# Optimization experiments

Measured on AMD Instinct MI355X. Metric: run time of the kernel, lower is better.

## Reference

```python
import jax, jax.numpy as jnp
import numpy as np

B, D, O = 8192, 64, 256

def setup_inputs() -> dict:
    key = jax.random.key(0)
    k1, k2, k3 = jax.random.split(key, 3)
    x = jax.random.normal(k1, (B, D), dtype=jnp.float32)
    centers = jax.random.uniform(k2, (O, 1, D), dtype=jnp.float32)  # RandomUniform(0,1)
    # Original uses Constant(10.0) which saturates exp(-quad) to 0; use small random
    # betas so the quadratic form is in a numerically meaningful range.
    betas = jax.random.normal(k3, (O, D, D), dtype=jnp.float32) * 0.05
    return {"x": x, "centers": centers, "betas": betas}

def reference(x, centers, betas):
    # precision[o] = betas[o] @ betas[o]^T   -> [O, D, D]
    precision = jnp.einsum('ode,ofe->odf', betas, betas)
    # diff[o,b,:] = centers[o] - x[b]        -> [O, B, D]
    diff = centers - x[None, :, :]
    # quad[o,b] = diff[o,b]^T P[o] diff[o,b] -> [O, B]
    quad = jnp.einsum('obd,odf,obf->ob', diff, precision, diff)
    return jnp.exp(-quad).T  # [B, O]
```

## Files before the change

kernel.cpp:

```cpp
#include <hip/hip_runtime.h>
#include <hip/hip_bf16.h>

typedef __bf16 bf16x8 __attribute__((ext_vector_type(8)));
typedef __bf16 bf16x4 __attribute__((ext_vector_type(4)));
typedef float  f32x4  __attribute__((ext_vector_type(4)));

constexpr int Bn = 8192, Dn = 64, On = 256;

__global__ void k_prep_beta(const float* __restrict__ betas, const float* __restrict__ centers,
                            __bf16* __restrict__ bT, float* __restrict__ cproj) {
    __shared__ float s[64 * 65];
    const int o = blockIdx.x, tid = threadIdx.x;
    const float* bo = betas + (size_t)o * 4096;
    for (int j = tid; j < 1024; j += 256) {
        int d = j >> 4, e = (j & 15) * 4;
        float4 v = ((const float4*)bo)[j];
        s[d * 65 + e + 0] = v.x; s[d * 65 + e + 1] = v.y;
        s[d * 65 + e + 2] = v.z; s[d * 65 + e + 3] = v.w;
    }
    __syncthreads();
    for (int j = tid; j < 1024; j += 256) {
        int e = j >> 4, d = (j & 15) * 4;
        bf16x4 r;
        r[0] = (__bf16)s[(d + 0) * 65 + e]; r[1] = (__bf16)s[(d + 1) * 65 + e];
        r[2] = (__bf16)s[(d + 2) * 65 + e]; r[3] = (__bf16)s[(d + 3) * 65 + e];
        *(bf16x4*)(bT + (size_t)o * 4096 + e * 64 + d) = r;
    }
    if (tid < 64) {
        float acc = 0.f;
        for (int d = 0; d < 64; ++d) acc += s[d * 65 + tid] * centers[o * 64 + d];
        cproj[o * 64 + tid] = acc;
    }
}

__global__ __launch_bounds__(256, 3) void k_main(const float* __restrict__ x,
                                                 const __bf16* __restrict__ bT,
                                                 const float* __restrict__ cproj,
                                                 float* __restrict__ out) {
    __shared__ __align__(16) unsigned char smem[256 * 144 + 256 * 8 * 4];
    __bf16* sX = (__bf16*)smem;
    float*  sQ = (float*)(smem + 256 * 144);

    const int tid  = threadIdx.x;
    const int w    = tid >> 6, lane = tid & 63;
    const int col  = lane & 15, grp = lane >> 4;
    const int ob   = blockIdx.x;
    const int bbase = blockIdx.y * 256;

#pragma unroll
    for (int it = 0; it < 16; ++it) {
        int i = it * 256 + tid;
        int row = i >> 4, q4 = i & 15;
        float4 v = ((const float4*)(x + (size_t)(bbase + row) * 64))[q4];
        bf16x4 r;
        r[0] = (__bf16)v.x; r[1] = (__bf16)v.y; r[2] = (__bf16)v.z; r[3] = (__bf16)v.w;
        *(bf16x4*)(sX + row * 72 + q4 * 4) = r;
    }

    const int o0 = ob * 8 + w * 2;
    bf16x8 A[2][4][2];
    f32x4  cpv[2][4];
#pragma unroll
    for (int o2 = 0; o2 < 2; ++o2) {
        const __bf16* bo = bT + (size_t)(o0 + o2) * 4096 + (size_t)col * 64 + grp * 8;
        const float*  cp = cproj + (o0 + o2) * 64 + grp * 4;
#pragma unroll
        for (int mi = 0; mi < 4; ++mi) {
            A[o2][mi][0] = *(const bf16x8*)(bo + mi * 16 * 64);
            A[o2][mi][1] = *(const bf16x8*)(bo + mi * 16 * 64 + 32);
            cpv[o2][mi]  = *(const f32x4*)(cp + mi * 16);
        }
    }
    __syncthreads();

#pragma unroll
    for (int n = 0; n < 16; ++n) {
        const __bf16* xr = sX + (n * 16 + col) * 72 + grp * 8;
        bf16x8 x0 = *(const bf16x8*)(xr);
        bf16x8 x1 = *(const bf16x8*)(xr + 32);
#pragma unroll
        for (int o2 = 0; o2 < 2; ++o2) {
            f32x4 qv = {0.f, 0.f, 0.f, 0.f};
#pragma unroll
            for (int mi = 0; mi < 4; ++mi) {
                f32x4 acc = {0.f, 0.f, 0.f, 0.f};
                acc = __builtin_amdgcn_mfma_f32_16x16x32_bf16(A[o2][mi][0], x0, acc, 0, 0, 0);
                acc = __builtin_amdgcn_mfma_f32_16x16x32_bf16(A[o2][mi][1], x1, acc, 0, 0, 0);
                f32x4 t = cpv[o2][mi] - acc;
                qv += t * t;
            }
            float qs = (qv[0] + qv[1]) + (qv[2] + qv[3]);
            qs += __shfl_xor(qs, 16, 64);
            qs += __shfl_xor(qs, 32, 64);
            if (grp == o2) sQ[(n * 16 + col) * 8 + w * 2 + o2] = qs;
        }
    }
    __syncthreads();

    f32x4 q0 = *(const f32x4*)(sQ + tid * 8);
    f32x4 q1 = *(const f32x4*)(sQ + tid * 8 + 4);
    f32x4 r0, r1;
#pragma unroll
    for (int j = 0; j < 4; ++j) { r0[j] = __expf(-q0[j]); r1[j] = __expf(-q1[j]); }
    float* op = out + (size_t)(bbase + tid) * 256 + ob * 8;
    *(f32x4*)op       = r0;
    *(f32x4*)(op + 4) = r1;
}

extern "C" void kernel_launch(void* const* d_in, const int* in_sizes, int n_in,
                              void* d_out, int out_size, void* d_ws, size_t ws_size,
                              hipStream_t stream) {
    const float* x       = (const float*)d_in[0];
    const float* centers = (const float*)d_in[1];
    const float* betas   = (const float*)d_in[2];
    float* out = (float*)d_out;

    char* ws = (char*)d_ws;
    __bf16* bT  = (__bf16*)ws;
    float*  cpj = (float*)(ws + 2 * (1 << 20));

    k_prep_beta<<<dim3(On),                dim3(256), 0, stream>>>(betas, centers, bT, cpj);
    k_main     <<<dim3(On / 8, Bn / 256),  dim3(256), 0, stream>>>(x, bT, cpj, out);
}
```

Before: 90.08 us.

## Give each wave one output, fold centre projection into MFMA accumulator, drop shuffles

Each wave now handles a single output index instead of two. The negated centre projection seeds the MFMA accumulator, so the subtraction disappears. Cross-lane shuffle reductions are replaced by writing partial sums to shared memory and reducing them during the exp/store phase. The grid is reordered so the batch is the fast dimension, shared memory is reused for the partial sums, and the occupancy hint rises to 4 blocks. In exchange each block stages the x tile twice as often per output and stores narrower 16-byte output rows.

```diff
diff --git a/kernel.cpp b/kernel.cpp
--- a/kernel.cpp
+++ b/kernel.cpp
@@ -8,7 +8,7 @@
 constexpr int Bn = 8192, Dn = 64, On = 256;
 
 __global__ void k_prep_beta(const float* __restrict__ betas, const float* __restrict__ centers,
-                            __bf16* __restrict__ bT, float* __restrict__ cproj) {
+                            __bf16* __restrict__ bT, float* __restrict__ ncproj) {
     __shared__ float s[64 * 65];
     const int o = blockIdx.x, tid = threadIdx.x;
     const float* bo = betas + (size_t)o * 4096;
@@ -29,23 +29,34 @@
     if (tid < 64) {
         float acc = 0.f;
         for (int d = 0; d < 64; ++d) acc += s[d * 65 + tid] * centers[o * 64 + d];
-        cproj[o * 64 + tid] = acc;
+        ncproj[o * 64 + tid] = -acc;
     }
 }
 
-__global__ __launch_bounds__(256, 3) void k_main(const float* __restrict__ x,
+__global__ __launch_bounds__(256, 4) void k_main(const float* __restrict__ x,
                                                  const __bf16* __restrict__ bT,
-                                                 const float* __restrict__ cproj,
+                                                 const float* __restrict__ ncproj,
                                                  float* __restrict__ out) {
-    __shared__ __align__(16) unsigned char smem[256 * 144 + 256 * 8 * 4];
+    __shared__ __align__(16) unsigned char smem[256 * 144];
     __bf16* sX = (__bf16*)smem;
-    float*  sQ = (float*)(smem + 256 * 144);
+    float*  sQ = (float*)smem;
 
     const int tid  = threadIdx.x;
     const int w    = tid >> 6, lane = tid & 63;
     const int col  = lane & 15, grp = lane >> 4;
-    const int ob   = blockIdx.x;
-    const int bbase = blockIdx.y * 256;
+    const int bbase = blockIdx.x * 256;
+    const int o     = blockIdx.y * 4 + w;
+
+    const __bf16* bo = bT + (size_t)o * 4096 + (size_t)col * 64 + grp * 8;
+    const float*  cp = ncproj + o * 64 + grp * 4;
+    bf16x8 A[4][2];
+    f32x4  ncp[4];
+#pragma unroll
+    for (int mi = 0; mi < 4; ++mi) {
+        A[mi][0] = *(const bf16x8*)(bo + mi * 16 * 64);
+        A[mi][1] = *(const bf16x8*)(bo + mi * 16 * 64 + 32);
+        ncp[mi]  = *(const f32x4*)(cp + mi * 16);
+    }
 
 #pragma unroll
     for (int it = 0; it < 16; ++it) {
@@ -56,55 +67,39 @@
         r[0] = (__bf16)v.x; r[1] = (__bf16)v.y; r[2] = (__bf16)v.z; r[3] = (__bf16)v.w;
         *(bf16x4*)(sX + row * 72 + q4 * 4) = r;
     }
-
-    const int o0 = ob * 8 + w * 2;
-    bf16x8 A[2][4][2];
-    f32x4  cpv[2][4];
-#pragma unroll
-    for (int o2 = 0; o2 < 2; ++o2) {
-        const __bf16* bo = bT + (size_t)(o0 + o2) * 4096 + (size_t)col * 64 + grp * 8;
-        const float*  cp = cproj + (o0 + o2) * 64 + grp * 4;
-#pragma unroll
-        for (int mi = 0; mi < 4; ++mi) {
-            A[o2][mi][0] = *(const bf16x8*)(bo + mi * 16 * 64);
-            A[o2][mi][1] = *(const bf16x8*)(bo + mi * 16 * 64 + 32);
-            cpv[o2][mi]  = *(const f32x4*)(cp + mi * 16);
-        }
-    }
     __syncthreads();
 
+    float qp[16];
 #pragma unroll
     for (int n = 0; n < 16; ++n) {
         const __bf16* xr = sX + (n * 16 + col) * 72 + grp * 8;
         bf16x8 x0 = *(const bf16x8*)(xr);
         bf16x8 x1 = *(const bf16x8*)(xr + 32);
+        f32x4 qv = {0.f, 0.f, 0.f, 0.f};
 #pragma unroll
-        for (int o2 = 0; o2 < 2; ++o2) {
-            f32x4 qv = {0.f, 0.f, 0.f, 0.f};
-#pragma unroll
-            for (int mi = 0; mi < 4; ++mi) {
-                f32x4 acc = {0.f, 0.f, 0.f, 0.f};
-                acc = __builtin_amdgcn_mfma_f32_16x16x32_bf16(A[o2][mi][0], x0, acc, 0, 0, 0);
-                acc = __builtin_amdgcn_mfma_f32_16x16x32_bf16(A[o2][mi][1], x1, acc, 0, 0, 0);
-                f32x4 t = cpv[o2][mi] - acc;
-                qv += t * t;
-            }
-            float qs = (qv[0] + qv[1]) + (qv[2] + qv[3]);
-            qs += __shfl_xor(qs, 16, 64);
-            qs += __shfl_xor(qs, 32, 64);
-            if (grp == o2) sQ[(n * 16 + col) * 8 + w * 2 + o2] = qs;
+        for (int mi = 0; mi < 4; ++mi) {
+            f32x4 acc = ncp[mi];
+            acc = __builtin_amdgcn_mfma_f32_16x16x32_bf16(A[mi][0], x0, acc, 0, 0, 0);
+            acc = __builtin_amdgcn_mfma_f32_16x16x32_bf16(A[mi][1], x1, acc, 0, 0, 0);
+            qv += acc * acc;
         }
+        qp[n] = (qv[0] + qv[1]) + (qv[2] + qv[3]);
     }
     __syncthreads();
 
-    f32x4 q0 = *(const f32x4*)(sQ + tid * 8);
-    f32x4 q1 = *(const f32x4*)(sQ + tid * 8 + 4);
-    f32x4 r0, r1;
 #pragma unroll
-    for (int j = 0; j < 4; ++j) { r0[j] = __expf(-q0[j]); r1[j] = __expf(-q1[j]); }
-    float* op = out + (size_t)(bbase + tid) * 256 + ob * 8;
-    *(f32x4*)op       = r0;
-    *(f32x4*)(op + 4) = r1;
+    for (int n = 0; n < 16; ++n)
+        sQ[(n * 16 + col) * 20 + w * 4 + grp] = qp[n];
+    __syncthreads();
+
+    const float* qr = sQ + tid * 20;
+    f32x4 r;
+#pragma unroll
+    for (int j = 0; j < 4; ++j) {
+        f32x4 v = *(const f32x4*)(qr + j * 4);
+        r[j] = __expf(-((v[0] + v[1]) + (v[2] + v[3])));
+    }
+    *(f32x4*)(out + (size_t)(bbase + tid) * 256 + blockIdx.y * 4) = r;
 }
 
 extern "C" void kernel_launch(void* const* d_in, const int* in_sizes, int n_in,
@@ -116,9 +111,9 @@
     float* out = (float*)d_out;
 
     char* ws = (char*)d_ws;
-    __bf16* bT  = (__bf16*)ws;
-    float*  cpj = (float*)(ws + 2 * (1 << 20));
+    __bf16* bT   = (__bf16*)ws;
+    float*  ncpj = (float*)(ws + 2 * (1 << 20));
 
-    k_prep_beta<<<dim3(On),                dim3(256), 0, stream>>>(betas, centers, bT, cpj);
-    k_main     <<<dim3(On / 8, Bn / 256),  dim3(256), 0, stream>>>(x, bT, cpj, out);
+    k_prep_beta<<<dim3(On),               dim3(256), 0, stream>>>(betas, centers, bT, ncpj);
+    k_main     <<<dim3(Bn / 256, On / 4), dim3(256), 0, stream>>>(x, bT, ncpj, out);
 }
```

New measurement: 93.25 us. 3.5% more time.
